# Kernel tuning notes

Measured on AMD Instinct MI355X. Metric: run time of the kernel, lower is better.

Reference implementation:

```python
import jax, jax.numpy as jnp
import numpy as np

NUM_HEADS = 16


def setup_inputs() -> dict:
    key = jax.random.key(0)
    ks = jax.random.split(key, 5)
    b, s, d = 2, 2048, 1024
    std = (2.0 / (d + d)) ** 0.5
    x = jax.random.normal(ks[0], (b, s, d), dtype=jnp.float32)
    Wq = jax.random.normal(ks[1], (d, d), dtype=jnp.float32) * std
    Wk = jax.random.normal(ks[2], (d, d), dtype=jnp.float32) * std
    Wv = jax.random.normal(ks[3], (d, d), dtype=jnp.float32) * std
    Wo = jax.random.normal(ks[4], (d, d), dtype=jnp.float32) * std
    return {"x": x, "Wq": Wq, "Wk": Wk, "Wv": Wv, "Wo": Wo}


def reference(x, Wq, Wk, Wv, Wo):
    b, s, d = x.shape
    h = NUM_HEADS
    dk = d // h
    # projections: bias-free x @ W (W is [in, out])
    def split_heads(t):
        return t.reshape(b, s, h, dk).transpose(0, 2, 1, 3)  # b h s dk
    q = split_heads(x @ Wq)
    k = split_heads(x @ Wk)
    v = split_heads(x @ Wv)
    scale = 1.0 / jnp.sqrt(jnp.asarray(dk, dtype=x.dtype))
    scores = jnp.einsum('bhqd,bhkd->bhqk', q, k) * scale  # b h s s
    causal = jnp.tril(jnp.ones((s, s), dtype=bool))
    scores = jnp.where(causal, scores, -jnp.inf)
    probs = jax.nn.softmax(scores, axis=-1)
    out = jnp.einsum('bhqk,bhkd->bhqd', probs, v)
    out = out.transpose(0, 2, 1, 3).reshape(b, s, d)  # b s (h dk)
    return out @ Wo
```

## Files before the change

### kernel.cpp

```cpp
#include <hip/hip_runtime.h>

typedef unsigned short u16;
typedef unsigned int   u32;

using bf16x8 = __attribute__((ext_vector_type(8))) __bf16;
using f32x4  = __attribute__((ext_vector_type(4))) float;
using s16x4  = __attribute__((ext_vector_type(4))) short;

#define NH    16
#define DKH   64
#define SEQ   2048
#define BAT   2
#define DMOD  1024

#define QSCALE 0.18033688011112042f

__device__ __forceinline__ u16 f2bf(float f) {
  union { float f; u32 u; } v; v.f = f;
  u32 r = v.u + 0x7fffu + ((v.u >> 16) & 1u);
  return (u16)(r >> 16);
}

__device__ __forceinline__ u32 pack2bf(float a, float b) {
  union { float f; u32 u; } x, y; x.f = a; y.f = b;
  u32 ua = x.u + 0x7fffu + ((x.u >> 16) & 1u);
  u32 ub = y.u + 0x7fffu + ((y.u >> 16) & 1u);
  return __builtin_amdgcn_perm(ub, ua, 0x07060302u);
}

#if __has_builtin(__builtin_amdgcn_exp2f)
#define EXP2(x) __builtin_amdgcn_exp2f(x)
#else
#define EXP2(x) exp2f(x)
#endif

#if __has_builtin(__builtin_amdgcn_mfma_f32_16x16x16bf16_1k)
__device__ __forceinline__ f32x4 mfma16(s16x4 a, s16x4 b, f32x4 c) {
  return __builtin_amdgcn_mfma_f32_16x16x16bf16_1k(a, b, c, 0, 0, 0);
}
#else
__device__ __forceinline__ f32x4 mfma16(s16x4 a, s16x4 b, f32x4 c) {
  f32x4 d;
  asm volatile("v_mfma_f32_16x16x16_bf16 %0, %1, %2, %3\n\ts_nop 7\n\ts_nop 7"
               : "=v"(d) : "v"(a), "v"(b), "v"(c));
  return d;
}
#endif

__global__ __launch_bounds__(256) void transpose_all(const float* __restrict__ Wq,
                                                     const float* __restrict__ Wk,
                                                     const float* __restrict__ Wv,
                                                     const float* __restrict__ Wo,
                                                     u16* __restrict__ Wt) {
  __shared__ u16 t[32][33];
  const float* W = blockIdx.z == 0 ? Wq : blockIdx.z == 1 ? Wk : blockIdx.z == 2 ? Wv : Wo;
  u16* o = Wt + (size_t)blockIdx.z * DMOD * DMOD;
  int bx = blockIdx.x * 32, by = blockIdx.y * 32;
  int x = threadIdx.x, y = threadIdx.y;
  #pragma unroll
  for (int i = 0; i < 32; i += 8)
    t[y + i][x] = f2bf(W[(size_t)(by + y + i) * DMOD + bx + x]);
  __syncthreads();
  #pragma unroll
  for (int i = 0; i < 32; i += 8)
    o[(size_t)(bx + y + i) * DMOD + by + x] = t[x][y + i];
}

__global__ __launch_bounds__(256) void convert_x(const float* __restrict__ x,
                                                 u16* __restrict__ xb) {
  size_t i = ((size_t)blockIdx.x * 256 + threadIdx.x) * 8;
  float4 f0 = *(const float4*)(x + i);
  float4 f1 = *(const float4*)(x + i + 4);
  uint4 o;
  o.x = pack2bf(f0.x, f0.y); o.y = pack2bf(f0.z, f0.w);
  o.z = pack2bf(f1.x, f1.y); o.w = pack2bf(f1.z, f1.w);
  *(uint4*)(xb + i) = o;
}

__global__ __launch_bounds__(256, 3) void gemm_qkv(const u16* __restrict__ A,
                                                   const u16* __restrict__ Bt,
                                                   u16* __restrict__ Qo,
                                                   u16* __restrict__ Ko,
                                                   u16* __restrict__ Vo) {
  __shared__ __align__(16) u16 As[128 * 40];
  __shared__ __align__(16) u16 Bs[128 * 40];
  const int tid  = threadIdx.x;
  const int lane = tid & 63, wv = tid >> 6;
  const int wm   = wv >> 1, wn = wv & 1;
  const int lrow = lane & 15, quad = lane >> 4;
  const int tileM = blockIdx.x * 128, tileN = blockIdx.y * 128;
  const int r0 = tid >> 2, c0 = (tid & 3) * 8;
  const int r1 = r0 + 64;

  const f32x4 fz = {0.f, 0.f, 0.f, 0.f};
  f32x4 acc[4][4];
  #pragma unroll
  for (int i = 0; i < 4; ++i)
    #pragma unroll
    for (int j = 0; j < 4; ++j) acc[i][j] = fz;

  uint4 a0 = *(const uint4*)(&A [(size_t)(tileM + r0) * DMOD + c0]);
  uint4 a1 = *(const uint4*)(&A [(size_t)(tileM + r1) * DMOD + c0]);
  uint4 b0 = *(const uint4*)(&Bt[(size_t)(tileN + r0) * DMOD + c0]);
  uint4 b1 = *(const uint4*)(&Bt[(size_t)(tileN + r1) * DMOD + c0]);

  for (int kt = 0; kt < DMOD; kt += 32) {
    __syncthreads();
    *(uint4*)(&As[r0 * 40 + c0]) = a0;
    *(uint4*)(&As[r1 * 40 + c0]) = a1;
    *(uint4*)(&Bs[r0 * 40 + c0]) = b0;
    *(uint4*)(&Bs[r1 * 40 + c0]) = b1;
    if (kt + 32 < DMOD) {
      a0 = *(const uint4*)(&A [(size_t)(tileM + r0) * DMOD + kt + 32 + c0]);
      a1 = *(const uint4*)(&A [(size_t)(tileM + r1) * DMOD + kt + 32 + c0]);
      b0 = *(const uint4*)(&Bt[(size_t)(tileN + r0) * DMOD + kt + 32 + c0]);
      b1 = *(const uint4*)(&Bt[(size_t)(tileN + r1) * DMOD + kt + 32 + c0]);
    }
    __syncthreads();
    bf16x8 af[4], bfr[4];
    #pragma unroll
    for (int mt = 0; mt < 4; ++mt)
      af[mt] = *(const bf16x8*)(&As[(wm * 64 + mt * 16 + lrow) * 40 + quad * 8]);
    #pragma unroll
    for (int nt = 0; nt < 4; ++nt)
      bfr[nt] = *(const bf16x8*)(&Bs[(wn * 64 + nt * 16 + lrow) * 40 + quad * 8]);
    #pragma unroll
    for (int mt = 0; mt < 4; ++mt)
      #pragma unroll
      for (int nt = 0; nt < 4; ++nt)
        acc[mt][nt] = __builtin_amdgcn_mfma_f32_16x16x32_bf16(af[mt], bfr[nt],
                                                              acc[mt][nt], 0, 0, 0);
  }

  #pragma unroll
  for (int mt = 0; mt < 4; ++mt) {
    #pragma unroll
    for (int nt = 0; nt < 4; ++nt) {
      int gm0 = tileM + wm * 64 + mt * 16 + quad * 4;
      int gn  = tileN + wn * 64 + nt * 16 + lrow;
      int which = gn >> 10, col = gn & 1023;
      int bb = gm0 >> 11, srw0 = gm0 & (SEQ - 1);
      int hh = col >> 6, dki = col & (DKH - 1);
      size_t bhi = (size_t)(bb * NH + hh);
      if (which == 0) {
        #pragma unroll
        for (int r = 0; r < 4; ++r)
          Qo[(bhi * SEQ + srw0 + r) * DKH + dki] = f2bf(acc[mt][nt][r] * QSCALE);
      } else if (which == 1) {
        #pragma unroll
        for (int r = 0; r < 4; ++r)
          Ko[(bhi * SEQ + srw0 + r) * DKH + dki] = f2bf(acc[mt][nt][r]);
      } else {
        uint2 pk;
        pk.x = pack2bf(acc[mt][nt][0], acc[mt][nt][1]);
        pk.y = pack2bf(acc[mt][nt][2], acc[mt][nt][3]);
        *(uint2*)(&Vo[(((bhi * (SEQ / 4)) + (srw0 >> 2)) * DKH + dki) * 4]) = pk;
      }
    }
  }
}

__global__ __launch_bounds__(256, 3) void gemm_out(const u16* __restrict__ A,
                                                   const u16* __restrict__ Bt,
                                                   float* __restrict__ Co) {
  __shared__ __align__(16) u16 As[128 * 40];
  __shared__ __align__(16) u16 Bs[64 * 40];
  const int tid  = threadIdx.x;
  const int lane = tid & 63, wv = tid >> 6;
  const int wm   = wv & 1, wn = wv >> 1;
  const int lrow = lane & 15, quad = lane >> 4;
  const int tileM = blockIdx.x * 128, tileN = blockIdx.y * 64;
  const int r0 = tid >> 2, c0 = (tid & 3) * 8;
  const int r1 = r0 + 64;

  const f32x4 fz = {0.f, 0.f, 0.f, 0.f};
  f32x4 acc[4][2];
  #pragma unroll
  for (int i = 0; i < 4; ++i) { acc[i][0] = fz; acc[i][1] = fz; }

  uint4 a0 = *(const uint4*)(&A [(size_t)(tileM + r0) * DMOD + c0]);
  uint4 a1 = *(const uint4*)(&A [(size_t)(tileM + r1) * DMOD + c0]);
  uint4 b0 = *(const uint4*)(&Bt[(size_t)(tileN + (r0 & 63)) * DMOD + c0]);

  for (int kt = 0; kt < DMOD; kt += 32) {
    __syncthreads();
    *(uint4*)(&As[r0 * 40 + c0]) = a0;
    *(uint4*)(&As[r1 * 40 + c0]) = a1;
    if (r0 < 64) *(uint4*)(&Bs[r0 * 40 + c0]) = b0;
    if (kt + 32 < DMOD) {
      a0 = *(const uint4*)(&A [(size_t)(tileM + r0) * DMOD + kt + 32 + c0]);
      a1 = *(const uint4*)(&A [(size_t)(tileM + r1) * DMOD + kt + 32 + c0]);
      b0 = *(const uint4*)(&Bt[(size_t)(tileN + (r0 & 63)) * DMOD + kt + 32 + c0]);
    }
    __syncthreads();
    bf16x8 af[4], bfr[2];
    #pragma unroll
    for (int mt = 0; mt < 4; ++mt)
      af[mt] = *(const bf16x8*)(&As[(wm * 64 + mt * 16 + lrow) * 40 + quad * 8]);
    #pragma unroll
    for (int nt = 0; nt < 2; ++nt)
      bfr[nt] = *(const bf16x8*)(&Bs[(wn * 32 + nt * 16 + lrow) * 40 + quad * 8]);
    #pragma unroll
    for (int mt = 0; mt < 4; ++mt)
      #pragma unroll
      for (int nt = 0; nt < 2; ++nt)
        acc[mt][nt] = __builtin_amdgcn_mfma_f32_16x16x32_bf16(af[mt], bfr[nt],
                                                              acc[mt][nt], 0, 0, 0);
  }

  #pragma unroll
  for (int mt = 0; mt < 4; ++mt)
    #pragma unroll
    for (int nt = 0; nt < 2; ++nt)
      #pragma unroll
      for (int r = 0; r < 4; ++r) {
        int gm = tileM + wm * 64 + mt * 16 + quad * 4 + r;
        int gn = tileN + wn * 32 + nt * 16 + lrow;
        Co[(size_t)gm * DMOD + gn] = acc[mt][nt][r];
      }
}

#define KP 72
#define VP 132
#define OP 72

__global__ __launch_bounds__(512) void attn_k(const u16* __restrict__ Q,
                                              const u16* __restrict__ Kg,
                                              const u16* __restrict__ Vg,
                                              u16* __restrict__ Og) {
  __shared__ __align__(16) u16 KsA[128 * KP];
  __shared__ __align__(16) u16 VsA[64 * VP];
  __shared__ __align__(16) u16 KsB[128 * KP];
  __shared__ __align__(16) u16 VsB[64 * VP];
  __shared__ __align__(16) u16 Os[128 * OP];

  const int tid  = threadIdx.x;
  const int lane = tid & 63, w = tid >> 6;
  const int lrow = lane & 15, quad = lane >> 4;
  const int bh = blockIdx.x, pr = blockIdx.y;
  const int b = bh >> 4, h = bh & 15;

  const u16* Qbh = Q  + (size_t)bh * SEQ * DKH;
  const u16* Kbh = Kg + (size_t)bh * SEQ * DKH;
  const u16* Vbh = Vg + (size_t)bh * SEQ * DKH;

  uint4 kreg[2], vreg[2];
  #pragma unroll
  for (int k = 0; k < 2; ++k) {
    int ci = k * 512 + tid;
    kreg[k] = *(const uint4*)(&Kbh[(size_t)(ci >> 3) * DKH + (ci & 7) * 8]);
    vreg[k] = *(const uint4*)(&Vbh[(size_t)(ci >> 5) * 256 + (ci & 31) * 8]);
  }

  int cur = 0;
  const f32x4 fz = {0.f, 0.f, 0.f, 0.f};

  for (int half = 0; half < 2; ++half) {
    const int qt = half ? (15 - pr) : pr;
    const int jmax = qt;
    const int qglob = qt * 128 + w * 16 + lrow;

    bf16x8 bq[2];
    #pragma unroll
    for (int kk = 0; kk < 2; ++kk)
      bq[kk] = *(const bf16x8*)(&Qbh[(size_t)qglob * DKH + kk * 32 + quad * 8]);

    f32x4 oacc[4];
    #pragma unroll
    for (int d = 0; d < 4; ++d) oacc[d] = fz;
    float lsum = 0.f;

    for (int j = 0; j <= jmax; ++j) {
      u16* Ks = cur ? KsB : KsA;
      u16* Vs = cur ? VsB : VsA;

      #pragma unroll
      for (int k = 0; k < 2; ++k) {
        int ci = k * 512 + tid;
        *(uint4*)(&Ks[(ci >> 3) * KP + (ci & 7) * 8]) = kreg[k];
        int sq = ci >> 5, dkp = ci & 31;
        union { uint4 q; uint2 d[2]; } vv; vv.q = vreg[k];
        *(uint2*)(&Vs[(2 * dkp)     * VP + 4 * sq]) = vv.d[0];
        *(uint2*)(&Vs[(2 * dkp + 1) * VP + 4 * sq]) = vv.d[1];
      }

      const bool pf = (j < jmax) || (half == 0);
      if (pf) {
        const int jn = (j < jmax) ? (j + 1) : 0;
        #pragma unroll
        for (int k = 0; k < 2; ++k) {
          int ci = k * 512 + tid;
          kreg[k] = *(const uint4*)(&Kbh[(size_t)(jn * 128 + (ci >> 3)) * DKH + (ci & 7) * 8]);
          vreg[k] = *(const uint4*)(&Vbh[(size_t)(jn * 32 + (ci >> 5)) * 256 + (ci & 31) * 8]);
        }
      }

      __syncthreads();

      if (j < jmax) {
        f32x4 sacc[8];
        #pragma unroll
        for (int m = 0; m < 8; ++m) sacc[m] = fz;
        #pragma unroll
        for (int kk = 0; kk < 2; ++kk)
          #pragma unroll
          for (int m = 0; m < 8; ++m) {
            bf16x8 ak = *(const bf16x8*)(&Ks[(m * 16 + lrow) * KP + kk * 32 + quad * 8]);
            sacc[m] = __builtin_amdgcn_mfma_f32_16x16x32_bf16(ak, bq[kk], sacc[m], 0, 0, 0);
          }
        #pragma unroll
        for (int m = 0; m < 8; ++m)
          #pragma unroll
          for (int r = 0; r < 4; ++r) {
            float p = EXP2(sacc[m][r]);
            sacc[m][r] = p;
            lsum += p;
          }
        #pragma unroll
        for (int m = 0; m < 8; ++m) {
          union { u32 u[2]; s16x4 v; } pk;
          pk.u[0] = pack2bf(sacc[m][0], sacc[m][1]);
          pk.u[1] = pack2bf(sacc[m][2], sacc[m][3]);
          #pragma unroll
          for (int d = 0; d < 4; ++d) {
            s16x4 av = *(const s16x4*)(&Vs[(d * 16 + lrow) * VP + m * 16 + quad * 4]);
            oacc[d] = mfma16(av, pk.v, oacc[d]);
          }
        }
      } else {
        for (int m = 0; m < w; ++m) {
          f32x4 s = fz;
          #pragma unroll
          for (int kk = 0; kk < 2; ++kk) {
            bf16x8 ak = *(const bf16x8*)(&Ks[(m * 16 + lrow) * KP + kk * 32 + quad * 8]);
            s = __builtin_amdgcn_mfma_f32_16x16x32_bf16(ak, bq[kk], s, 0, 0, 0);
          }
          union { u32 u[2]; s16x4 v; } pk;
          float p0 = EXP2(s[0]), p1 = EXP2(s[1]), p2 = EXP2(s[2]), p3 = EXP2(s[3]);
          lsum += (p0 + p1) + (p2 + p3);
          pk.u[0] = pack2bf(p0, p1);
          pk.u[1] = pack2bf(p2, p3);
          #pragma unroll
          for (int d = 0; d < 4; ++d) {
            s16x4 av = *(const s16x4*)(&Vs[(d * 16 + lrow) * VP + m * 16 + quad * 4]);
            oacc[d] = mfma16(av, pk.v, oacc[d]);
          }
        }
        {
          f32x4 s = fz;
          #pragma unroll
          for (int kk = 0; kk < 2; ++kk) {
            bf16x8 ak = *(const bf16x8*)(&Ks[(w * 16 + lrow) * KP + kk * 32 + quad * 8]);
            s = __builtin_amdgcn_mfma_f32_16x16x32_bf16(ak, bq[kk], s, 0, 0, 0);
          }
          float p[4];
          #pragma unroll
          for (int r = 0; r < 4; ++r) {
            int kg = jmax * 128 + w * 16 + quad * 4 + r;
            p[r] = (kg > qglob) ? 0.f : EXP2(s[r]);
            lsum += p[r];
          }
          union { u32 u[2]; s16x4 v; } pk;
          pk.u[0] = pack2bf(p[0], p[1]);
          pk.u[1] = pack2bf(p[2], p[3]);
          #pragma unroll
          for (int d = 0; d < 4; ++d) {
            s16x4 av = *(const s16x4*)(&Vs[(d * 16 + lrow) * VP + w * 16 + quad * 4]);
            oacc[d] = mfma16(av, pk.v, oacc[d]);
          }
        }
      }
      cur ^= 1;
    }

    float ls = lsum;
    ls += __shfl_xor(ls, 16, 64);
    ls += __shfl_xor(ls, 32, 64);
    float inv = 1.f / ls;

    #pragma unroll
    for (int d = 0; d < 4; ++d) {
      uint2 pk;
      pk.x = pack2bf(oacc[d][0] * inv, oacc[d][1] * inv);
      pk.y = pack2bf(oacc[d][2] * inv, oacc[d][3] * inv);
      *(uint2*)(&Os[(w * 16 + lrow) * OP + d * 16 + quad * 4]) = pk;
    }
    __syncthreads();
    #pragma unroll
    for (int k = 0; k < 2; ++k) {
      int c = k * 512 + tid;
      int row = c >> 3, ch = c & 7;
      uint4 v = *(const uint4*)(&Os[row * OP + ch * 8]);
      *(uint4*)(&Og[(size_t)(b * SEQ + qt * 128 + row) * DMOD + h * DKH + ch * 8]) = v;
    }
    __syncthreads();
  }
}

extern "C" void kernel_launch(void* const* d_in, const int* in_sizes, int n_in,
                              void* d_out, int out_size, void* d_ws, size_t ws_size,
                              hipStream_t stream) {
  const float* x  = (const float*)d_in[0];
  const float* Wq = (const float*)d_in[1];
  const float* Wk = (const float*)d_in[2];
  const float* Wv = (const float*)d_in[3];
  const float* Wo = (const float*)d_in[4];

  u16* ws = (u16*)d_ws;
  const size_t WSZ = (size_t)DMOD * DMOD;
  const size_t TSZ = (size_t)BAT * NH * SEQ * DKH;
  u16* Wt  = ws;
  u16* Wto = Wt + 3 * WSZ;
  u16* xb  = Wt + 4 * WSZ;
  u16* Qb  = xb + TSZ;
  u16* Kb  = Qb + TSZ;
  u16* Vb  = Kb + TSZ;
  u16* Ob  = xb;

  transpose_all<<<dim3(32, 32, 4), dim3(32, 8), 0, stream>>>(Wq, Wk, Wv, Wo, Wt);
  convert_x<<<dim3(2048), 256, 0, stream>>>(x, xb);

  gemm_qkv<<<dim3(32, 24), 256, 0, stream>>>(xb, Wt, Qb, Kb, Vb);

  attn_k<<<dim3(32, 8), 512, 0, stream>>>(Qb, Kb, Vb, Ob);

  gemm_out<<<dim3(32, 16), 256, 0, stream>>>(Ob, Wto, (float*)d_out);
}
```

Baseline: 180.8 us.

## Split paired causal tiles into separate blocks with two query strips per wave

The attention kernel no longer pairs query tiles pr and 15-pr inside one 512-thread block. Instead it launches 16 tiles per head as 256-thread blocks, with each wave handling two 16-row query strips so every K/V fragment load from shared memory feeds two MFMAs. The output staging buffer in shared memory is removed and results are written straight to global memory. This raises the block count and cuts LDS reads per MFMA, but block work is now imbalanced across causal tiles, register pressure rises, and global stores become narrower.

```diff
diff --git a/kernel.cpp b/kernel.cpp
--- a/kernel.cpp
+++ b/kernel.cpp
@@ -222,178 +222,173 @@
 
 #define KP 72
 #define VP 132
-#define OP 72
-
-__global__ __launch_bounds__(512) void attn_k(const u16* __restrict__ Q,
-                                              const u16* __restrict__ Kg,
-                                              const u16* __restrict__ Vg,
-                                              u16* __restrict__ Og) {
+
+__global__ __launch_bounds__(256, 2) void attn_k(const u16* __restrict__ Q,
+                                                 const u16* __restrict__ Kg,
+                                                 const u16* __restrict__ Vg,
+                                                 u16* __restrict__ Og) {
   __shared__ __align__(16) u16 KsA[128 * KP];
   __shared__ __align__(16) u16 VsA[64 * VP];
   __shared__ __align__(16) u16 KsB[128 * KP];
   __shared__ __align__(16) u16 VsB[64 * VP];
-  __shared__ __align__(16) u16 Os[128 * OP];
 
   const int tid  = threadIdx.x;
   const int lane = tid & 63, w = tid >> 6;
   const int lrow = lane & 15, quad = lane >> 4;
-  const int bh = blockIdx.x, pr = blockIdx.y;
+  const int bh = blockIdx.x;
+  const int t  = blockIdx.y;
+  const int qt = (t < 8) ? t : 23 - t;
   const int b = bh >> 4, h = bh & 15;
 
   const u16* Qbh = Q  + (size_t)bh * SEQ * DKH;
   const u16* Kbh = Kg + (size_t)bh * SEQ * DKH;
   const u16* Vbh = Vg + (size_t)bh * SEQ * DKH;
 
-  uint4 kreg[2], vreg[2];
-  #pragma unroll
-  for (int k = 0; k < 2; ++k) {
-    int ci = k * 512 + tid;
+  const int jmax = qt;
+
+  bf16x8 bq[2][2];
+  #pragma unroll
+  for (int s = 0; s < 2; ++s)
+    #pragma unroll
+    for (int kk = 0; kk < 2; ++kk)
+      bq[s][kk] = *(const bf16x8*)(&Qbh[(size_t)(qt * 128 + (2 * w + s) * 16 + lrow) * DKH
+                                        + kk * 32 + quad * 8]);
+
+  uint4 kreg[4], vreg[4];
+  #pragma unroll
+  for (int k = 0; k < 4; ++k) {
+    int ci = k * 256 + tid;
     kreg[k] = *(const uint4*)(&Kbh[(size_t)(ci >> 3) * DKH + (ci & 7) * 8]);
     vreg[k] = *(const uint4*)(&Vbh[(size_t)(ci >> 5) * 256 + (ci & 31) * 8]);
   }
 
+  const f32x4 fz = {0.f, 0.f, 0.f, 0.f};
+  f32x4 oacc[2][4];
+  #pragma unroll
+  for (int s = 0; s < 2; ++s)
+    #pragma unroll
+    for (int d = 0; d < 4; ++d) oacc[s][d] = fz;
+  float lsum[2] = {0.f, 0.f};
+
   int cur = 0;
-  const f32x4 fz = {0.f, 0.f, 0.f, 0.f};
-
-  for (int half = 0; half < 2; ++half) {
-    const int qt = half ? (15 - pr) : pr;
-    const int jmax = qt;
-    const int qglob = qt * 128 + w * 16 + lrow;
-
-    bf16x8 bq[2];
-    #pragma unroll
-    for (int kk = 0; kk < 2; ++kk)
-      bq[kk] = *(const bf16x8*)(&Qbh[(size_t)qglob * DKH + kk * 32 + quad * 8]);
-
-    f32x4 oacc[4];
-    #pragma unroll
-    for (int d = 0; d < 4; ++d) oacc[d] = fz;
-    float lsum = 0.f;
-
-    for (int j = 0; j <= jmax; ++j) {
-      u16* Ks = cur ? KsB : KsA;
-      u16* Vs = cur ? VsB : VsA;
-
-      #pragma unroll
-      for (int k = 0; k < 2; ++k) {
-        int ci = k * 512 + tid;
-        *(uint4*)(&Ks[(ci >> 3) * KP + (ci & 7) * 8]) = kreg[k];
-        int sq = ci >> 5, dkp = ci & 31;
-        union { uint4 q; uint2 d[2]; } vv; vv.q = vreg[k];
-        *(uint2*)(&Vs[(2 * dkp)     * VP + 4 * sq]) = vv.d[0];
-        *(uint2*)(&Vs[(2 * dkp + 1) * VP + 4 * sq]) = vv.d[1];
+  for (int j = 0; j <= jmax; ++j) {
+    u16* Ks = cur ? KsB : KsA;
+    u16* Vs = cur ? VsB : VsA;
+
+    #pragma unroll
+    for (int k = 0; k < 4; ++k) {
+      int ci = k * 256 + tid;
+      *(uint4*)(&Ks[(ci >> 3) * KP + (ci & 7) * 8]) = kreg[k];
+      int sq = ci >> 5, dkp = ci & 31;
+      union { uint4 q; uint2 d[2]; } vv; vv.q = vreg[k];
+      *(uint2*)(&Vs[(2 * dkp)     * VP + 4 * sq]) = vv.d[0];
+      *(uint2*)(&Vs[(2 * dkp + 1) * VP + 4 * sq]) = vv.d[1];
+    }
+
+    if (j < jmax) {
+      const int jn = j + 1;
+      #pragma unroll
+      for (int k = 0; k < 4; ++k) {
+        int ci = k * 256 + tid;
+        kreg[k] = *(const uint4*)(&Kbh[(size_t)(jn * 128 + (ci >> 3)) * DKH + (ci & 7) * 8]);
+        vreg[k] = *(const uint4*)(&Vbh[(size_t)(jn * 32 + (ci >> 5)) * 256 + (ci & 31) * 8]);
       }
-
-      const bool pf = (j < jmax) || (half == 0);
-      if (pf) {
-        const int jn = (j < jmax) ? (j + 1) : 0;
+    }
+
+    __syncthreads();
+
+    if (j < jmax) {
+      f32x4 sacc[2][8];
+      #pragma unroll
+      for (int s = 0; s < 2; ++s)
         #pragma unroll
-        for (int k = 0; k < 2; ++k) {
-          int ci = k * 512 + tid;
-          kreg[k] = *(const uint4*)(&Kbh[(size_t)(jn * 128 + (ci >> 3)) * DKH + (ci & 7) * 8]);
-          vreg[k] = *(const uint4*)(&Vbh[(size_t)(jn * 32 + (ci >> 5)) * 256 + (ci & 31) * 8]);
+        for (int m = 0; m < 8; ++m) sacc[s][m] = fz;
+      #pragma unroll
+      for (int kk = 0; kk < 2; ++kk)
+        #pragma unroll
+        for (int m = 0; m < 8; ++m) {
+          bf16x8 ak = *(const bf16x8*)(&Ks[(m * 16 + lrow) * KP + kk * 32 + quad * 8]);
+          sacc[0][m] = __builtin_amdgcn_mfma_f32_16x16x32_bf16(ak, bq[0][kk], sacc[0][m], 0, 0, 0);
+          sacc[1][m] = __builtin_amdgcn_mfma_f32_16x16x32_bf16(ak, bq[1][kk], sacc[1][m], 0, 0, 0);
+        }
+      #pragma unroll
+      for (int m = 0; m < 8; ++m) {
+        float p00 = EXP2(sacc[0][m][0]), p01 = EXP2(sacc[0][m][1]);
+        float p02 = EXP2(sacc[0][m][2]), p03 = EXP2(sacc[0][m][3]);
+        float p10 = EXP2(sacc[1][m][0]), p11 = EXP2(sacc[1][m][1]);
+        float p12 = EXP2(sacc[1][m][2]), p13 = EXP2(sacc[1][m][3]);
+        lsum[0] += (p00 + p01) + (p02 + p03);
+        lsum[1] += (p10 + p11) + (p12 + p13);
+        union { u32 u[2]; s16x4 v; } pk0, pk1;
+        pk0.u[0] = pack2bf(p00, p01); pk0.u[1] = pack2bf(p02, p03);
+        pk1.u[0] = pack2bf(p10, p11); pk1.u[1] = pack2bf(p12, p13);
+        #pragma unroll
+        for (int d = 0; d < 4; ++d) {
+          s16x4 av = *(const s16x4*)(&Vs[(d * 16 + lrow) * VP + m * 16 + quad * 4]);
+          oacc[0][d] = mfma16(av, pk0.v, oacc[0][d]);
+          oacc[1][d] = mfma16(av, pk1.v, oacc[1][d]);
         }
       }
-
-      __syncthreads();
-
-      if (j < jmax) {
-        f32x4 sacc[8];
-        #pragma unroll
-        for (int m = 0; m < 8; ++m) sacc[m] = fz;
-        #pragma unroll
-        for (int kk = 0; kk < 2; ++kk)
+    } else {
+      #pragma unroll
+      for (int s = 0; s < 2; ++s) {
+        const int ws = 2 * w + s;
+        for (int m = 0; m < ws; ++m) {
+          f32x4 sv = fz;
           #pragma unroll
-          for (int m = 0; m < 8; ++m) {
+          for (int kk = 0; kk < 2; ++kk) {
             bf16x8 ak = *(const bf16x8*)(&Ks[(m * 16 + lrow) * KP + kk * 32 + quad * 8]);
-            sacc[m] = __builtin_amdgcn_mfma_f32_16x16x32_bf16(ak, bq[kk], sacc[m], 0, 0, 0);
+            sv = __builtin_amdgcn_mfma_f32_16x16x32_bf16(ak, bq[s][kk], sv, 0, 0, 0);
           }
-        #pragma unroll
-        for (int m = 0; m < 8; ++m)
-          #pragma unroll
-          for (int r = 0; r < 4; ++r) {
-            float p = EXP2(sacc[m][r]);
-            sacc[m][r] = p;
-            lsum += p;
-          }
-        #pragma unroll
-        for (int m = 0; m < 8; ++m) {
+          float p0 = EXP2(sv[0]), p1 = EXP2(sv[1]), p2 = EXP2(sv[2]), p3 = EXP2(sv[3]);
+          lsum[s] += (p0 + p1) + (p2 + p3);
           union { u32 u[2]; s16x4 v; } pk;
-          pk.u[0] = pack2bf(sacc[m][0], sacc[m][1]);
-          pk.u[1] = pack2bf(sacc[m][2], sacc[m][3]);
+          pk.u[0] = pack2bf(p0, p1); pk.u[1] = pack2bf(p2, p3);
           #pragma unroll
           for (int d = 0; d < 4; ++d) {
             s16x4 av = *(const s16x4*)(&Vs[(d * 16 + lrow) * VP + m * 16 + quad * 4]);
-            oacc[d] = mfma16(av, pk.v, oacc[d]);
-          }
-        }
-      } else {
-        for (int m = 0; m < w; ++m) {
-          f32x4 s = fz;
-          #pragma unroll
-          for (int kk = 0; kk < 2; ++kk) {
-            bf16x8 ak = *(const bf16x8*)(&Ks[(m * 16 + lrow) * KP + kk * 32 + quad * 8]);
-            s = __builtin_amdgcn_mfma_f32_16x16x32_bf16(ak, bq[kk], s, 0, 0, 0);
-          }
-          union { u32 u[2]; s16x4 v; } pk;
-          float p0 = EXP2(s[0]), p1 = EXP2(s[1]), p2 = EXP2(s[2]), p3 = EXP2(s[3]);
-          lsum += (p0 + p1) + (p2 + p3);
-          pk.u[0] = pack2bf(p0, p1);
-          pk.u[1] = pack2bf(p2, p3);
-          #pragma unroll
-          for (int d = 0; d < 4; ++d) {
-            s16x4 av = *(const s16x4*)(&Vs[(d * 16 + lrow) * VP + m * 16 + quad * 4]);
-            oacc[d] = mfma16(av, pk.v, oacc[d]);
+            oacc[s][d] = mfma16(av, pk.v, oacc[s][d]);
           }
         }
         {
-          f32x4 s = fz;
+          f32x4 sv = fz;
           #pragma unroll
           for (int kk = 0; kk < 2; ++kk) {
-            bf16x8 ak = *(const bf16x8*)(&Ks[(w * 16 + lrow) * KP + kk * 32 + quad * 8]);
-            s = __builtin_amdgcn_mfma_f32_16x16x32_bf16(ak, bq[kk], s, 0, 0, 0);
+            bf16x8 ak = *(const bf16x8*)(&Ks[(ws * 16 + lrow) * KP + kk * 32 + quad * 8]);
+            sv = __builtin_amdgcn_mfma_f32_16x16x32_bf16(ak, bq[s][kk], sv, 0, 0, 0);
           }
           float p[4];
           #pragma unroll
-          for (int r = 0; r < 4; ++r) {
-            int kg = jmax * 128 + w * 16 + quad * 4 + r;
-            p[r] = (kg > qglob) ? 0.f : EXP2(s[r]);
-            lsum += p[r];
-          }
+          for (int r = 0; r < 4; ++r)
+            p[r] = (quad * 4 + r > lrow) ? 0.f : EXP2(sv[r]);
+          lsum[s] += (p[0] + p[1]) + (p[2] + p[3]);
           union { u32 u[2]; s16x4 v; } pk;
-          pk.u[0] = pack2bf(p[0], p[1]);
-          pk.u[1] = pack2bf(p[2], p[3]);
+          pk.u[0] = pack2bf(p[0], p[1]); pk.u[1] = pack2bf(p[2], p[3]);
           #pragma unroll
           for (int d = 0; d < 4; ++d) {
-            s16x4 av = *(const s16x4*)(&Vs[(d * 16 + lrow) * VP + w * 16 + quad * 4]);
-            oacc[d] = mfma16(av, pk.v, oacc[d]);
+            s16x4 av = *(const s16x4*)(&Vs[(d * 16 + lrow) * VP + ws * 16 + quad * 4]);
+            oacc[s][d] = mfma16(av, pk.v, oacc[s][d]);
           }
         }
       }
-      cur ^= 1;
-    }
-
-    float ls = lsum;
+    }
+    cur ^= 1;
+  }
+
+  #pragma unroll
+  for (int s = 0; s < 2; ++s) {
+    float ls = lsum[s];
     ls += __shfl_xor(ls, 16, 64);
     ls += __shfl_xor(ls, 32, 64);
     float inv = 1.f / ls;
-
+    int qrow = qt * 128 + (2 * w + s) * 16 + lrow;
     #pragma unroll
     for (int d = 0; d < 4; ++d) {
-      uint2 pk;
-      pk.x = pack2bf(oacc[d][0] * inv, oacc[d][1] * inv);
-      pk.y = pack2bf(oacc[d][2] * inv, oacc[d][3] * inv);
-      *(uint2*)(&Os[(w * 16 + lrow) * OP + d * 16 + quad * 4]) = pk;
-    }
-    __syncthreads();
-    #pragma unroll
-    for (int k = 0; k < 2; ++k) {
-      int c = k * 512 + tid;
-      int row = c >> 3, ch = c & 7;
-      uint4 v = *(const uint4*)(&Os[row * OP + ch * 8]);
-      *(uint4*)(&Og[(size_t)(b * SEQ + qt * 128 + row) * DMOD + h * DKH + ch * 8]) = v;
-    }
-    __syncthreads();
+      uint2 pkk;
+      pkk.x = pack2bf(oacc[s][d][0] * inv, oacc[s][d][1] * inv);
+      pkk.y = pack2bf(oacc[s][d][2] * inv, oacc[s][d][3] * inv);
+      *(uint2*)(&Og[(size_t)(b * SEQ + qrow) * DMOD + h * DKH + d * 16 + quad * 4]) = pkk;
+    }
   }
 }
 
@@ -422,7 +417,7 @@
 
   gemm_qkv<<<dim3(32, 24), 256, 0, stream>>>(xb, Wt, Qb, Kb, Vb);
 
-  attn_k<<<dim3(32, 8), 512, 0, stream>>>(Qb, Kb, Vb, Ob);
+  attn_k<<<dim3(32, 16), 256, 0, stream>>>(Qb, Kb, Vb, Ob);
 
   gemm_out<<<dim3(32, 16), 256, 0, stream>>>(Ob, Wto, (float*)d_out);
 }
```

New measurement: 177.9 us. No clear change (-1.6%).
